# Kernel optimization log

Hardware: AMD Instinct MI355X
Metric: run time of the kernel (lower is better)

## Reference

```python
import jax, jax.numpy as jnp
import numpy as np

EPS_LN1 = 1e-6   # partial(nn.LayerNorm, eps=1e-6)
EPS_OUT = 1e-5   # nn.LayerNorm default inside SS3D out_norm


def _layernorm(x, w, b, eps):
    m = jnp.mean(x, axis=-1, keepdims=True)
    v = jnp.var(x, axis=-1, keepdims=True)
    return (x - m) * jax.lax.rsqrt(v + eps) * w + b


def _selective_scan(dA, dBx):
    # dA, dBx: (B, K, d, L, N); linear recurrence h_t = dA_t * h_{t-1} + dBx_t
    def comb(c1, c2):
        a1, b1 = c1
        a2, b2 = c2
        return a2 * a1, a2 * b1 + b2
    _, hs = jax.lax.associative_scan(comb, (dA, dBx), axis=3)
    return hs  # (B, K, d, L, N)


def setup_inputs() -> dict:
    key = jax.random.key(0)
    ks = jax.random.split(key, 12)
    B, D, H, W, C = 1, 16, 16, 16, 96
    d, N, K, R = 96, 16, 6, 6  # d_inner, d_state, n_scan_dirs, dt_rank
    s = 0.02
    f = lambda k, shp: jax.random.normal(k, shp, dtype=jnp.float32)
    return {
        "x": f(ks[0], (B, D, H, W, C)),
        "ln1_w": jnp.ones((C,), jnp.float32),
        "ln1_b": jnp.zeros((C,), jnp.float32),
        "in_proj_w": f(ks[1], (2 * d, C)) * s,
        "conv_w": f(ks[2], (d, 1, 3, 3, 3)) * s,
        "conv_b": f(ks[3], (d,)) * s,
        "x_proj_w": f(ks[4], (K, R + 2 * N, d)) * s,
        "dt_proj_w": f(ks[5], (K, d, R)) * s,
        "dt_proj_b": f(ks[6], (K, d)) * s,
        "A_log": jnp.log(1.0 + 15.0 * jax.random.uniform(ks[7], (K, d, N), jnp.float32)),
        "D_skip": f(ks[8], (K, d)) * s,
        "out_norm_w": jnp.ones((d,), jnp.float32),
        "out_norm_b": jnp.zeros((d,), jnp.float32),
        "out_proj_w": f(ks[9], (C, d)) * s,
    }


def reference(x, ln1_w, ln1_b, in_proj_w, conv_w, conv_b, x_proj_w,
              dt_proj_w, dt_proj_b, A_log, D_skip, out_norm_w, out_norm_b,
              out_proj_w):
    B, D, H, W, C = x.shape
    L = D * H * W
    K, _, d = x_proj_w.shape
    R = dt_proj_w.shape[2]
    N = A_log.shape[2]

    # pre-norm
    xn = _layernorm(x, ln1_w, ln1_b, EPS_LN1)

    # in_proj -> (x, z)
    xz = jnp.einsum('bdhwc,ec->bdhwe', xn, in_proj_w)  # (B,D,H,W,2d)
    xh, z = jnp.split(xz, 2, axis=-1)

    # depthwise 3x3x3 conv + SiLU, channels-first
    xc = jnp.transpose(xh, (0, 4, 1, 2, 3))  # (B,d,D,H,W)
    xc = jax.lax.conv_general_dilated(
        xc, conv_w, window_strides=(1, 1, 1), padding='SAME',
        dimension_numbers=('NCDHW', 'OIDHW', 'NCDHW'),
        feature_group_count=d)
    xc = jax.nn.silu(xc + conv_b[None, :, None, None, None])

    # K = 6 scan orderings: DHW, HWD, WDH and their reverses
    o0 = xc.reshape(B, d, L)
    o1 = jnp.transpose(xc, (0, 1, 3, 4, 2)).reshape(B, d, L)  # (H,W,D) order
    o2 = jnp.transpose(xc, (0, 1, 4, 2, 3)).reshape(B, d, L)  # (W,D,H) order
    fwd3 = jnp.stack([o0, o1, o2], axis=1)                    # (B,3,d,L)
    xs = jnp.concatenate([fwd3, jnp.flip(fwd3, axis=-1)], axis=1)  # (B,K,d,L)

    # per-direction input-dependent parameters
    x_dbl = jnp.einsum('bkdl,kcd->bkcl', xs, x_proj_w)        # (B,K,R+2N,L)
    dt, Bm, Cm = jnp.split(x_dbl, [R, R + N], axis=2)
    dts = jnp.einsum('bkrl,kdr->bkdl', dt, dt_proj_w) + dt_proj_b[None, :, :, None]
    dts = jax.nn.softplus(dts)                                # delta_softplus

    A = -jnp.exp(A_log)                                       # (K,d,N)
    dA = jnp.exp(dts[..., None] * A[None, :, :, None, :])     # (B,K,d,L,N)
    Bt = jnp.transpose(Bm, (0, 1, 3, 2))                      # (B,K,L,N)
    dBx = (dts * xs)[..., None] * Bt[:, :, None, :, :]        # (B,K,d,L,N)

    hs = _selective_scan(dA, dBx)                             # (B,K,d,L,N)
    Ct = jnp.transpose(Cm, (0, 1, 3, 2))                      # (B,K,L,N)
    ys = jnp.einsum('bkdln,bkln->bkdl', hs, Ct) + D_skip[None, :, :, None] * xs

    # undo reversals and orderings, sum the 6 paths
    yf = ys[:, :3] + jnp.flip(ys[:, 3:], axis=-1)             # (B,3,d,L)
    y0 = yf[:, 0]
    y1 = jnp.transpose(yf[:, 1].reshape(B, d, H, W, D), (0, 1, 4, 2, 3)).reshape(B, d, L)
    y2 = jnp.transpose(yf[:, 2].reshape(B, d, W, D, H), (0, 1, 3, 4, 2)).reshape(B, d, L)
    y = (y0 + y1 + y2).reshape(B, d, D, H, W)
    y = jnp.transpose(y, (0, 2, 3, 4, 1))                     # (B,D,H,W,d)

    # out_norm, gate, out_proj
    y = _layernorm(y, out_norm_w, out_norm_b, EPS_OUT)
    y = y * jax.nn.silu(z)
    out = jnp.einsum('bdhwe,ce->bdhwc', y, out_proj_w)

    # residual (drop_path is identity at eval)
    return x + out
```

## Files before the change

### kernel.cpp

```cpp
#include <hip/hip_runtime.h>
#include <hip/hip_bf16.h>

#define L 4096
#define CDIM 96
#define DDIM 96
#define KDIR 6
#define NST 16
#define RRK 6
#define YSTRIDE 40
#define NCHUNK 256
#define CHLEN 16

typedef _Float16 half4v __attribute__((ext_vector_type(4)));

__device__ __forceinline__ float sigmoidf_(float x) { return 1.f / (1.f + __expf(-x)); }

__device__ __forceinline__ int sigma_k(int kb, int l) {
    if (kb == 0) return l;
    if (kb == 1) return ((l & 15) << 8) | ((l >> 8) << 4) | ((l >> 4) & 15);
    return (((l >> 4) & 15) << 8) | ((l & 15) << 4) | (l >> 8);
}

__global__ void __launch_bounds__(192) k1_ln_inproj(
        const float* __restrict__ x, const float* __restrict__ ln_w,
        const float* __restrict__ ln_b, const float* __restrict__ Wp,
        float* __restrict__ xh_t, float* __restrict__ zs) {
    int s0 = blockIdx.x * 8;
    int tid = threadIdx.x;
    __shared__ __align__(16) float xt[8][96];
    __shared__ __align__(16) float xn[8][96];
    __shared__ float mss[8], rss[8];
    ((float4*)&xt[0][0])[tid] = ((const float4*)(x + (size_t)s0 * 96))[tid];
    __syncthreads();
    int wave = tid >> 6, lane = tid & 63;
    for (int r = wave; r < 8; r += 3) {
        float v = xt[r][lane] + ((lane < 32) ? xt[r][64 + lane] : 0.f);
#pragma unroll
        for (int off = 1; off < 64; off <<= 1) v += __shfl_xor(v, off);
        float vs = xt[r][lane] * xt[r][lane] + ((lane < 32) ? xt[r][64 + lane] * xt[r][64 + lane] : 0.f);
#pragma unroll
        for (int off = 1; off < 64; off <<= 1) vs += __shfl_xor(vs, off);
        if (lane == 0) {
            float mean = v * (1.f / 96.f);
            float var = vs * (1.f / 96.f) - mean * mean;
            mss[r] = mean; rss[r] = rsqrtf(var + 1e-6f);
        }
    }
    __syncthreads();
    {
        int r = tid / 24, c4 = tid % 24;
        float4 xv = ((float4*)&xt[r][0])[c4];
        float4 wv = ((const float4*)ln_w)[c4];
        float4 bv = ((const float4*)ln_b)[c4];
        float m = mss[r], rs = rss[r];
        float4 o;
        o.x = (xv.x - m) * rs * wv.x + bv.x;
        o.y = (xv.y - m) * rs * wv.y + bv.y;
        o.z = (xv.z - m) * rs * wv.z + bv.z;
        o.w = (xv.w - m) * rs * wv.w + bv.w;
        ((float4*)&xn[r][0])[c4] = o;
    }
    float4 Wr[24];
    const float4* wr = (const float4*)(Wp + (size_t)tid * 96);
#pragma unroll
    for (int c4 = 0; c4 < 24; c4++) Wr[c4] = wr[c4];
    __syncthreads();
#pragma unroll
    for (int s = 0; s < 8; s++) {
        const float4* xr4 = (const float4*)&xn[s][0];
        float a0 = 0.f, a1 = 0.f, a2 = 0.f, a3 = 0.f;
#pragma unroll
        for (int c4 = 0; c4 < 24; c4 += 4) {
            float4 x0 = xr4[c4], x1 = xr4[c4 + 1], x2 = xr4[c4 + 2], x3 = xr4[c4 + 3];
            a0 += Wr[c4].x * x0.x + Wr[c4].y * x0.y + Wr[c4].z * x0.z + Wr[c4].w * x0.w;
            a1 += Wr[c4+1].x * x1.x + Wr[c4+1].y * x1.y + Wr[c4+1].z * x1.z + Wr[c4+1].w * x1.w;
            a2 += Wr[c4+2].x * x2.x + Wr[c4+2].y * x2.y + Wr[c4+2].z * x2.z + Wr[c4+2].w * x2.w;
            a3 += Wr[c4+3].x * x3.x + Wr[c4+3].y * x3.y + Wr[c4+3].z * x3.z + Wr[c4+3].w * x3.w;
        }
        float acc = (a0 + a1) + (a2 + a3);
        if (tid < 96) xh_t[(size_t)tid * L + s0 + s] = acc;
        else zs[(size_t)(s0 + s) * 96 + (tid - 96)] = acc * sigmoidf_(acc);
    }
}

__global__ void k2_conv(const float* __restrict__ xh_t, const float* __restrict__ cw,
                        const float* __restrict__ cb, float* __restrict__ xc,
                        float* __restrict__ xcT) {
    int idx = blockIdx.x * 256 + threadIdx.x;
    int c = idx >> 12, s = idx & 4095;
    int dz = s >> 8, h = (s >> 4) & 15, w = s & 15;
    const float* xin = xh_t + c * L;
    const float* wc = cw + c * 27;
    float acc = cb[c];
#pragma unroll
    for (int i = 0; i < 3; i++) {
        int z2 = dz + i - 1; if ((unsigned)z2 > 15u) continue;
#pragma unroll
        for (int j = 0; j < 3; j++) {
            int h2 = h + j - 1; if ((unsigned)h2 > 15u) continue;
#pragma unroll
            for (int kk = 0; kk < 3; kk++) {
                int w2 = w + kk - 1; if ((unsigned)w2 > 15u) continue;
                acc += xin[z2 * 256 + h2 * 16 + w2] * wc[i * 9 + j * 3 + kk];
            }
        }
    }
    float r = acc * sigmoidf_(acc);
    xc[c * L + s] = r;
    xcT[s * 96 + c] = r;
}

__global__ void k3_xproj(const float* __restrict__ xc, const float* __restrict__ Wx,
                         const float* __restrict__ Wdt, const float* __restrict__ bdt,
                         float* __restrict__ Y2, float* __restrict__ Zs) {
    int k = blockIdx.x;
    int tid = threadIdx.x;
    int sbase = blockIdx.y * 256;
    int s = sbase + tid;
    int ch = blockIdx.z;
    int base = (ch < 2) ? ch * 10 : 20 + (ch - 2) * 9;
    int cnt = (ch < 2) ? 10 : 9;
    __shared__ float dts[256][6];
    float acc[10];
#pragma unroll
    for (int i = 0; i < 10; i++) acc[i] = 0.f;
    const float* wk = Wx + ((size_t)k * (RRK + 2 * NST) + base) * DDIM;
    for (int dd = 0; dd < 96; dd += 4) {
        float v[4];
#pragma unroll
        for (int j = 0; j < 4; j++) v[j] = xc[(dd + j) * L + s];
#pragma unroll
        for (int j = 0; j < 4; j++)
#pragma unroll
            for (int i = 0; i < 10; i++) acc[i] += wk[i * DDIM + dd + j] * v[j];
    }
    float* yo = Y2 + ((size_t)k * L + s) * YSTRIDE;
#pragma unroll
    for (int i = 0; i < 10; i++) {
        if (i < cnt) {
            int c = base + i;
            if (c >= 6) yo[c + 2] = acc[i];
        }
    }
    if (ch == 0) {
#pragma unroll
        for (int r = 0; r < 6; r++) dts[tid][r] = acc[r];
        __syncthreads();
        for (int i = 0; i < 96; i++) {
            int idx = i * 256 + tid;
            int d = idx % 96;
            int sr = idx / 96;
            const float* wr = Wdt + ((size_t)k * 96 + d) * 6;
            float a = bdt[k * 96 + d];
#pragma unroll
            for (int r = 0; r < 6; r++) a += wr[r] * dts[sr][r];
            float sp = (a > 15.f) ? a : __logf(1.f + __expf(a));
            Zs[((size_t)k * L + sbase + sr) * 96 + d] = sp;
        }
    }
}


__global__ void __launch_bounds__(256) ka_scan(
        const float* __restrict__ Zs, const float* __restrict__ xcT,
        const float* __restrict__ Y2, const float* __restrict__ A_log,
        _Float16* __restrict__ Aah, _Float16* __restrict__ Abh) {
    int t = blockIdx.x * 256 + threadIdx.x;
    int nq = t & 3;
    int q = t >> 2;
    int d = q % 96;
    int rest = q / 96;
    int chunk = rest % NCHUNK;
    int k = rest / NCHUNK;
    int kb = (k < 3) ? k : (k - 3);
    bool flip = (k >= 3);
    float An[4];
    {
        float4 al = *(const float4*)(A_log + ((size_t)k * 96 + d) * 16 + nq * 4);
        An[0] = -__expf(al.x); An[1] = -__expf(al.y);
        An[2] = -__expf(al.z); An[3] = -__expf(al.w);
    }
    float a[4] = {1.f, 1.f, 1.f, 1.f};
    float b[4] = {0.f, 0.f, 0.f, 0.f};
    const float* Zk = Zs + (size_t)k * L * 96;
    const float* Yk = Y2 + (size_t)k * L * YSTRIDE;
    int l0 = chunk * CHLEN;
    for (int i = 0; i < CHLEN; i += 4) {
        int sI[4]; float dt[4], xv[4]; float4 Bv[4];
#pragma unroll
        for (int j = 0; j < 4; j++) {
            int l = l0 + i + j;
            int lp = flip ? (4095 - l) : l;
            sI[j] = sigma_k(kb, lp);
        }
#pragma unroll
        for (int j = 0; j < 4; j++) {
            dt[j] = Zk[(size_t)sI[j] * 96 + d];
            xv[j] = xcT[(size_t)sI[j] * 96 + d];
            Bv[j] = *(const float4*)(Yk + (size_t)sI[j] * YSTRIDE + 8 + nq * 4);
        }
#pragma unroll
        for (int j = 0; j < 4; j++) {
            float dtx = dt[j] * xv[j];
            float e0 = __expf(dt[j] * An[0]);
            float e1 = __expf(dt[j] * An[1]);
            float e2 = __expf(dt[j] * An[2]);
            float e3 = __expf(dt[j] * An[3]);
            b[0] = e0 * b[0] + dtx * Bv[j].x; a[0] *= e0;
            b[1] = e1 * b[1] + dtx * Bv[j].y; a[1] *= e1;
            b[2] = e2 * b[2] + dtx * Bv[j].z; a[2] *= e2;
            b[3] = e3 * b[3] + dtx * Bv[j].w; a[3] *= e3;
        }
    }
    size_t o = (((size_t)k * NCHUNK + chunk) * 96 + d) * 16 + nq * 4;
    half4v ha, hb;
    ha.x = (_Float16)a[0]; ha.y = (_Float16)a[1]; ha.z = (_Float16)a[2]; ha.w = (_Float16)a[3];
    hb.x = (_Float16)b[0]; hb.y = (_Float16)b[1]; hb.z = (_Float16)b[2]; hb.w = (_Float16)b[3];
    *(half4v*)(Aah + o) = ha;
    *(half4v*)(Abh + o) = hb;
}

__global__ void __launch_bounds__(256) kb_combine(
        const _Float16* __restrict__ Aah, const _Float16* __restrict__ Abh,
        _Float16* __restrict__ Pbh) {
    int t = blockIdx.x * 256 + threadIdx.x;
    int n = t & 15;
    int rest = t >> 4;
    int d = rest % 96;
    int k = rest / 96;
    size_t base = ((size_t)k * NCHUNK * 96 + d) * 16 + n;
    const size_t cstride = 96 * 16;
    float rb = 0.f;
    for (int c0 = 0; c0 < NCHUNK; c0 += 16) {
        float av[16], bv[16];
#pragma unroll
        for (int j = 0; j < 16; j++) {
            av[j] = (float)Aah[base + (size_t)(c0 + j) * cstride];
            bv[j] = (float)Abh[base + (size_t)(c0 + j) * cstride];
        }
#pragma unroll
        for (int j = 0; j < 16; j++) {
            Pbh[base + (size_t)(c0 + j) * cstride] = (_Float16)rb;
            rb = av[j] * rb + bv[j];
        }
    }
}

__global__ void __launch_bounds__(256) kc_apply(
        const float* __restrict__ Zs, const float* __restrict__ xcT,
        const float* __restrict__ Y2, const float* __restrict__ A_log,
        const float* __restrict__ D_skip, const _Float16* __restrict__ Pbh,
        float* __restrict__ ys_buf) {
    int t = blockIdx.x * 256 + threadIdx.x;
    int nq = t & 3;
    int q = t >> 2;
    int d = q % 96;
    int rest = q / 96;
    int chunk = rest % NCHUNK;
    int k = rest / NCHUNK;
    int kb = (k < 3) ? k : (k - 3);
    bool flip = (k >= 3);
    float An[4];
    {
        float4 al = *(const float4*)(A_log + ((size_t)k * 96 + d) * 16 + nq * 4);
        An[0] = -__expf(al.x); An[1] = -__expf(al.y);
        An[2] = -__expf(al.z); An[3] = -__expf(al.w);
    }
    float Dk = D_skip[k * DDIM + d];
    float h[4];
    {
        half4v hp = *(const half4v*)(Pbh + (((size_t)k * NCHUNK + chunk) * 96 + d) * 16 + nq * 4);
        h[0] = (float)hp.x; h[1] = (float)hp.y; h[2] = (float)hp.z; h[3] = (float)hp.w;
    }
    const float* Zk = Zs + (size_t)k * L * 96;
    const float* Yk = Y2 + (size_t)k * L * YSTRIDE;
    float* ysk = ys_buf + (size_t)k * L * 96;
    int l0 = chunk * CHLEN;
    for (int i = 0; i < CHLEN; i += 4) {
        int sI[4]; float dt[4], xv[4]; float4 Bv[4], Cv[4];
#pragma unroll
        for (int j = 0; j < 4; j++) {
            int l = l0 + i + j;
            int lp = flip ? (4095 - l) : l;
            sI[j] = sigma_k(kb, lp);
        }
#pragma unroll
        for (int j = 0; j < 4; j++) {
            dt[j] = Zk[(size_t)sI[j] * 96 + d];
            xv[j] = xcT[(size_t)sI[j] * 96 + d];
            Bv[j] = *(const float4*)(Yk + (size_t)sI[j] * YSTRIDE + 8 + nq * 4);
            Cv[j] = *(const float4*)(Yk + (size_t)sI[j] * YSTRIDE + 24 + nq * 4);
        }
#pragma unroll
        for (int j = 0; j < 4; j++) {
            float dtx = dt[j] * xv[j];
            float e0 = __expf(dt[j] * An[0]);
            float e1 = __expf(dt[j] * An[1]);
            float e2 = __expf(dt[j] * An[2]);
            float e3 = __expf(dt[j] * An[3]);
            h[0] = e0 * h[0] + dtx * Bv[j].x;
            h[1] = e1 * h[1] + dtx * Bv[j].y;
            h[2] = e2 * h[2] + dtx * Bv[j].z;
            h[3] = e3 * h[3] + dtx * Bv[j].w;
            float p = h[0] * Cv[j].x + h[1] * Cv[j].y + h[2] * Cv[j].z + h[3] * Cv[j].w;
            p += __shfl_xor(p, 1);
            p += __shfl_xor(p, 2);
            if (nq == 0) ysk[(size_t)sI[j] * 96 + d] = p + Dk * xv[j];
        }
    }
}

__global__ void __launch_bounds__(192) k6_out(
        const float* __restrict__ ys_buf, const float* __restrict__ zs,
        const float* __restrict__ onw, const float* __restrict__ onb,
        const float* __restrict__ Wo, const float* __restrict__ x,
        float* __restrict__ out) {
    int s0 = blockIdx.x * 16;
    int tid = threadIdx.x;
    __shared__ __align__(16) float vt[16][96];
    __shared__ __align__(16) float gt[16][96];
    __shared__ float mss[16], rss[16];
#pragma unroll
    for (int j = 0; j < 8; j++) {
        int f = tid + j * 192;
        int sr = f / 96, c = f % 96;
        float v = 0.f;
#pragma unroll
        for (int k = 0; k < KDIR; k++)
            v += ys_buf[((size_t)k * L + s0 + sr) * 96 + c];
        vt[sr][c] = v;
    }
    __syncthreads();
    int wave = tid >> 6, lane = tid & 63;
    for (int r = wave; r < 16; r += 3) {
        float v = vt[r][lane] + ((lane < 32) ? vt[r][64 + lane] : 0.f);
#pragma unroll
        for (int off = 1; off < 64; off <<= 1) v += __shfl_xor(v, off);
        float vs = vt[r][lane] * vt[r][lane] + ((lane < 32) ? vt[r][64 + lane] * vt[r][64 + lane] : 0.f);
#pragma unroll
        for (int off = 1; off < 64; off <<= 1) vs += __shfl_xor(vs, off);
        if (lane == 0) {
            float mean = v * (1.f / 96.f);
            float var = vs * (1.f / 96.f) - mean * mean;
            mss[r] = mean; rss[r] = rsqrtf(var + 1e-5f);
        }
    }
    __syncthreads();
#pragma unroll
    for (int j = 0; j < 8; j++) {
        int f = tid + j * 192;
        int sr = f / 96, c = f % 96;
        float g = (vt[sr][c] - mss[sr]) * rss[sr] * onw[c] + onb[c];
        gt[sr][c] = g * zs[(size_t)(s0 + sr) * 96 + c];
    }
    int e = tid % 96, sg = tid / 96;
    float4 Wr[24];
    const float4* wr = (const float4*)(Wo + (size_t)e * 96);
#pragma unroll
    for (int c4 = 0; c4 < 24; c4++) Wr[c4] = wr[c4];
    __syncthreads();
#pragma unroll
    for (int j = 0; j < 8; j++) {
        int s = sg * 8 + j;
        const float4* g4 = (const float4*)&gt[s][0];
        float a0 = 0.f, a1 = 0.f, a2 = 0.f, a3 = 0.f;
#pragma unroll
        for (int c4 = 0; c4 < 24; c4 += 4) {
            float4 x0 = g4[c4], x1 = g4[c4 + 1], x2 = g4[c4 + 2], x3 = g4[c4 + 3];
            a0 += Wr[c4].x * x0.x + Wr[c4].y * x0.y + Wr[c4].z * x0.z + Wr[c4].w * x0.w;
            a1 += Wr[c4+1].x * x1.x + Wr[c4+1].y * x1.y + Wr[c4+1].z * x1.z + Wr[c4+1].w * x1.w;
            a2 += Wr[c4+2].x * x2.x + Wr[c4+2].y * x2.y + Wr[c4+2].z * x2.z + Wr[c4+2].w * x2.w;
            a3 += Wr[c4+3].x * x3.x + Wr[c4+3].y * x3.y + Wr[c4+3].z * x3.z + Wr[c4+3].w * x3.w;
        }
        float acc = (a0 + a1) + (a2 + a3) + x[(size_t)(s0 + s) * 96 + e];
        out[(size_t)(s0 + s) * 96 + e] = acc;
    }
}

extern "C" void kernel_launch(void* const* d_in, const int* in_sizes, int n_in,
                              void* d_out, int out_size, void* d_ws, size_t ws_size,
                              hipStream_t stream) {
    const float* x        = (const float*)d_in[0];
    const float* ln1_w    = (const float*)d_in[1];
    const float* ln1_b    = (const float*)d_in[2];
    const float* in_proj  = (const float*)d_in[3];
    const float* conv_w   = (const float*)d_in[4];
    const float* conv_b   = (const float*)d_in[5];
    const float* x_proj   = (const float*)d_in[6];
    const float* dt_w     = (const float*)d_in[7];
    const float* dt_b     = (const float*)d_in[8];
    const float* A_log    = (const float*)d_in[9];
    const float* D_skip   = (const float*)d_in[10];
    const float* onw      = (const float*)d_in[11];
    const float* onb      = (const float*)d_in[12];
    const float* out_w    = (const float*)d_in[13];
    float* out = (float*)d_out;

    float* xh_t = (float*)d_ws;
    float* zs   = xh_t + 96 * L;
    float* xc   = zs + 96 * L;
    float* xcT  = xc + 96 * L;
    float* Y2   = xcT + 96 * L;
    float* Zs   = Y2 + (size_t)KDIR * L * YSTRIDE;
    float* ysb  = Zs + (size_t)KDIR * L * DDIM;
    _Float16* Aah = (_Float16*)(ysb + (size_t)KDIR * L * DDIM);
    _Float16* Abh = Aah + (size_t)KDIR * NCHUNK * DDIM * NST;
    _Float16* Pbh = Abh + (size_t)KDIR * NCHUNK * DDIM * NST;

    k1_ln_inproj<<<dim3(L / 8), dim3(192), 0, stream>>>(x, ln1_w, ln1_b, in_proj, xh_t, zs);
    k2_conv<<<dim3(96 * L / 256), dim3(256), 0, stream>>>(xh_t, conv_w, conv_b, xc, xcT);
    k3_xproj<<<dim3(KDIR, 16, 4), dim3(256), 0, stream>>>(xc, x_proj, dt_w, dt_b, Y2, Zs);
    ka_scan<<<dim3(KDIR * NCHUNK * DDIM * 4 / 256), dim3(256), 0, stream>>>(Zs, xcT, Y2, A_log, Aah, Abh);
    kb_combine<<<dim3(KDIR * DDIM * NST / 256), dim3(256), 0, stream>>>(Aah, Abh, Pbh);
    kc_apply<<<dim3(KDIR * NCHUNK * DDIM * 4 / 256), dim3(256), 0, stream>>>(Zs, xcT, Y2, A_log, D_skip, Pbh, ysb);
    k6_out<<<dim3(L / 16), dim3(192), 0, stream>>>(ysb, zs, onw, onb, out_w, x, out);
}
```

Baseline: 194.7 us.

## Store intermediate activations in fp16 and interleave scan outputs per position

Result: faster. 189.9 us (-2.4%).

```diff
diff --git a/kernel.cpp b/kernel.cpp
--- a/kernel.cpp
+++ b/kernel.cpp
@@ -7,7 +7,7 @@
 #define KDIR 6
 #define NST 16
 #define RRK 6
-#define YSTRIDE 40
+#define YH 32
 #define NCHUNK 256
 #define CHLEN 16
 
@@ -24,7 +24,7 @@
 __global__ void __launch_bounds__(192) k1_ln_inproj(
         const float* __restrict__ x, const float* __restrict__ ln_w,
         const float* __restrict__ ln_b, const float* __restrict__ Wp,
-        float* __restrict__ xh_t, float* __restrict__ zs) {
+        _Float16* __restrict__ xhh, _Float16* __restrict__ zsh) {
     int s0 = blockIdx.x * 8;
     int tid = threadIdx.x;
     __shared__ __align__(16) float xt[8][96];
@@ -78,18 +78,18 @@
             a3 += Wr[c4+3].x * x3.x + Wr[c4+3].y * x3.y + Wr[c4+3].z * x3.z + Wr[c4+3].w * x3.w;
         }
         float acc = (a0 + a1) + (a2 + a3);
-        if (tid < 96) xh_t[(size_t)tid * L + s0 + s] = acc;
-        else zs[(size_t)(s0 + s) * 96 + (tid - 96)] = acc * sigmoidf_(acc);
-    }
-}
-
-__global__ void k2_conv(const float* __restrict__ xh_t, const float* __restrict__ cw,
-                        const float* __restrict__ cb, float* __restrict__ xc,
-                        float* __restrict__ xcT) {
+        if (tid < 96) xhh[(size_t)tid * L + s0 + s] = (_Float16)acc;
+        else zsh[(size_t)(s0 + s) * 96 + (tid - 96)] = (_Float16)(acc * sigmoidf_(acc));
+    }
+}
+
+__global__ void k2_conv(const _Float16* __restrict__ xhh, const float* __restrict__ cw,
+                        const float* __restrict__ cb, _Float16* __restrict__ xch,
+                        _Float16* __restrict__ xcTh) {
     int idx = blockIdx.x * 256 + threadIdx.x;
     int c = idx >> 12, s = idx & 4095;
     int dz = s >> 8, h = (s >> 4) & 15, w = s & 15;
-    const float* xin = xh_t + c * L;
+    const _Float16* xin = xhh + (size_t)c * L;
     const float* wc = cw + c * 27;
     float acc = cb[c];
 #pragma unroll
@@ -101,18 +101,19 @@
 #pragma unroll
             for (int kk = 0; kk < 3; kk++) {
                 int w2 = w + kk - 1; if ((unsigned)w2 > 15u) continue;
-                acc += xin[z2 * 256 + h2 * 16 + w2] * wc[i * 9 + j * 3 + kk];
+                acc += (float)xin[z2 * 256 + h2 * 16 + w2] * wc[i * 9 + j * 3 + kk];
             }
         }
     }
     float r = acc * sigmoidf_(acc);
-    xc[c * L + s] = r;
-    xcT[s * 96 + c] = r;
-}
-
-__global__ void k3_xproj(const float* __restrict__ xc, const float* __restrict__ Wx,
+    _Float16 hr = (_Float16)r;
+    xch[(size_t)c * L + s] = hr;
+    xcTh[(size_t)s * 96 + c] = hr;
+}
+
+__global__ void k3_xproj(const _Float16* __restrict__ xch, const float* __restrict__ Wx,
                          const float* __restrict__ Wdt, const float* __restrict__ bdt,
-                         float* __restrict__ Y2, float* __restrict__ Zs) {
+                         _Float16* __restrict__ Y2h, _Float16* __restrict__ Zsh) {
     int k = blockIdx.x;
     int tid = threadIdx.x;
     int sbase = blockIdx.y * 256;
@@ -128,18 +129,18 @@
     for (int dd = 0; dd < 96; dd += 4) {
         float v[4];
 #pragma unroll
-        for (int j = 0; j < 4; j++) v[j] = xc[(dd + j) * L + s];
+        for (int j = 0; j < 4; j++) v[j] = (float)xch[(size_t)(dd + j) * L + s];
 #pragma unroll
         for (int j = 0; j < 4; j++)
 #pragma unroll
             for (int i = 0; i < 10; i++) acc[i] += wk[i * DDIM + dd + j] * v[j];
     }
-    float* yo = Y2 + ((size_t)k * L + s) * YSTRIDE;
+    _Float16* yo = Y2h + ((size_t)k * L + s) * YH;
 #pragma unroll
     for (int i = 0; i < 10; i++) {
         if (i < cnt) {
             int c = base + i;
-            if (c >= 6) yo[c + 2] = acc[i];
+            if (c >= 6) yo[c - 6] = (_Float16)acc[i];
         }
     }
     if (ch == 0) {
@@ -155,15 +156,15 @@
 #pragma unroll
             for (int r = 0; r < 6; r++) a += wr[r] * dts[sr][r];
             float sp = (a > 15.f) ? a : __logf(1.f + __expf(a));
-            Zs[((size_t)k * L + sbase + sr) * 96 + d] = sp;
+            Zsh[((size_t)k * L + sbase + sr) * 96 + d] = (_Float16)sp;
         }
     }
 }
 
 
 __global__ void __launch_bounds__(256) ka_scan(
-        const float* __restrict__ Zs, const float* __restrict__ xcT,
-        const float* __restrict__ Y2, const float* __restrict__ A_log,
+        const _Float16* __restrict__ Zsh, const _Float16* __restrict__ xcTh,
+        const _Float16* __restrict__ Y2h, const float* __restrict__ A_log,
         _Float16* __restrict__ Aah, _Float16* __restrict__ Abh) {
     int t = blockIdx.x * 256 + threadIdx.x;
     int nq = t & 3;
@@ -182,11 +183,11 @@
     }
     float a[4] = {1.f, 1.f, 1.f, 1.f};
     float b[4] = {0.f, 0.f, 0.f, 0.f};
-    const float* Zk = Zs + (size_t)k * L * 96;
-    const float* Yk = Y2 + (size_t)k * L * YSTRIDE;
+    const _Float16* Zk = Zsh + (size_t)k * L * 96;
+    const _Float16* Yk = Y2h + (size_t)k * L * YH;
     int l0 = chunk * CHLEN;
     for (int i = 0; i < CHLEN; i += 4) {
-        int sI[4]; float dt[4], xv[4]; float4 Bv[4];
+        int sI[4]; float dt[4], xv[4]; half4v Bh[4];
 #pragma unroll
         for (int j = 0; j < 4; j++) {
             int l = l0 + i + j;
@@ -195,9 +196,9 @@
         }
 #pragma unroll
         for (int j = 0; j < 4; j++) {
-            dt[j] = Zk[(size_t)sI[j] * 96 + d];
-            xv[j] = xcT[(size_t)sI[j] * 96 + d];
-            Bv[j] = *(const float4*)(Yk + (size_t)sI[j] * YSTRIDE + 8 + nq * 4);
+            dt[j] = (float)Zk[(size_t)sI[j] * 96 + d];
+            xv[j] = (float)xcTh[(size_t)sI[j] * 96 + d];
+            Bh[j] = *(const half4v*)(Yk + (size_t)sI[j] * YH + nq * 4);
         }
 #pragma unroll
         for (int j = 0; j < 4; j++) {
@@ -206,10 +207,10 @@
             float e1 = __expf(dt[j] * An[1]);
             float e2 = __expf(dt[j] * An[2]);
             float e3 = __expf(dt[j] * An[3]);
-            b[0] = e0 * b[0] + dtx * Bv[j].x; a[0] *= e0;
-            b[1] = e1 * b[1] + dtx * Bv[j].y; a[1] *= e1;
-            b[2] = e2 * b[2] + dtx * Bv[j].z; a[2] *= e2;
-            b[3] = e3 * b[3] + dtx * Bv[j].w; a[3] *= e3;
+            b[0] = e0 * b[0] + dtx * (float)Bh[j].x; a[0] *= e0;
+            b[1] = e1 * b[1] + dtx * (float)Bh[j].y; a[1] *= e1;
+            b[2] = e2 * b[2] + dtx * (float)Bh[j].z; a[2] *= e2;
+            b[3] = e3 * b[3] + dtx * (float)Bh[j].w; a[3] *= e3;
         }
     }
     size_t o = (((size_t)k * NCHUNK + chunk) * 96 + d) * 16 + nq * 4;
@@ -247,10 +248,10 @@
 }
 
 __global__ void __launch_bounds__(256) kc_apply(
-        const float* __restrict__ Zs, const float* __restrict__ xcT,
-        const float* __restrict__ Y2, const float* __restrict__ A_log,
+        const _Float16* __restrict__ Zsh, const _Float16* __restrict__ xcTh,
+        const _Float16* __restrict__ Y2h, const float* __restrict__ A_log,
         const float* __restrict__ D_skip, const _Float16* __restrict__ Pbh,
-        float* __restrict__ ys_buf) {
+        _Float16* __restrict__ ysh) {
     int t = blockIdx.x * 256 + threadIdx.x;
     int nq = t & 3;
     int q = t >> 2;
@@ -272,12 +273,11 @@
         half4v hp = *(const half4v*)(Pbh + (((size_t)k * NCHUNK + chunk) * 96 + d) * 16 + nq * 4);
         h[0] = (float)hp.x; h[1] = (float)hp.y; h[2] = (float)hp.z; h[3] = (float)hp.w;
     }
-    const float* Zk = Zs + (size_t)k * L * 96;
-    const float* Yk = Y2 + (size_t)k * L * YSTRIDE;
-    float* ysk = ys_buf + (size_t)k * L * 96;
+    const _Float16* Zk = Zsh + (size_t)k * L * 96;
+    const _Float16* Yk = Y2h + (size_t)k * L * YH;
     int l0 = chunk * CHLEN;
     for (int i = 0; i < CHLEN; i += 4) {
-        int sI[4]; float dt[4], xv[4]; float4 Bv[4], Cv[4];
+        int sI[4]; float dt[4], xv[4]; half4v Bh[4], Ch[4];
 #pragma unroll
         for (int j = 0; j < 4; j++) {
             int l = l0 + i + j;
@@ -286,10 +286,10 @@
         }
 #pragma unroll
         for (int j = 0; j < 4; j++) {
-            dt[j] = Zk[(size_t)sI[j] * 96 + d];
-            xv[j] = xcT[(size_t)sI[j] * 96 + d];
-            Bv[j] = *(const float4*)(Yk + (size_t)sI[j] * YSTRIDE + 8 + nq * 4);
-            Cv[j] = *(const float4*)(Yk + (size_t)sI[j] * YSTRIDE + 24 + nq * 4);
+            dt[j] = (float)Zk[(size_t)sI[j] * 96 + d];
+            xv[j] = (float)xcTh[(size_t)sI[j] * 96 + d];
+            Bh[j] = *(const half4v*)(Yk + (size_t)sI[j] * YH + nq * 4);
+            Ch[j] = *(const half4v*)(Yk + (size_t)sI[j] * YH + 16 + nq * 4);
         }
 #pragma unroll
         for (int j = 0; j < 4; j++) {
@@ -298,41 +298,42 @@
             float e1 = __expf(dt[j] * An[1]);
             float e2 = __expf(dt[j] * An[2]);
             float e3 = __expf(dt[j] * An[3]);
-            h[0] = e0 * h[0] + dtx * Bv[j].x;
-            h[1] = e1 * h[1] + dtx * Bv[j].y;
-            h[2] = e2 * h[2] + dtx * Bv[j].z;
-            h[3] = e3 * h[3] + dtx * Bv[j].w;
-            float p = h[0] * Cv[j].x + h[1] * Cv[j].y + h[2] * Cv[j].z + h[3] * Cv[j].w;
+            h[0] = e0 * h[0] + dtx * (float)Bh[j].x;
+            h[1] = e1 * h[1] + dtx * (float)Bh[j].y;
+            h[2] = e2 * h[2] + dtx * (float)Bh[j].z;
+            h[3] = e3 * h[3] + dtx * (float)Bh[j].w;
+            float p = h[0] * (float)Ch[j].x + h[1] * (float)Ch[j].y
+                    + h[2] * (float)Ch[j].z + h[3] * (float)Ch[j].w;
             p += __shfl_xor(p, 1);
             p += __shfl_xor(p, 2);
-            if (nq == 0) ysk[(size_t)sI[j] * 96 + d] = p + Dk * xv[j];
+            if (nq == 0) ysh[((size_t)sI[j] * KDIR + k) * 96 + d] = (_Float16)(p + Dk * xv[j]);
         }
     }
 }
 
 __global__ void __launch_bounds__(192) k6_out(
-        const float* __restrict__ ys_buf, const float* __restrict__ zs,
+        const _Float16* __restrict__ ysh, const _Float16* __restrict__ zsh,
         const float* __restrict__ onw, const float* __restrict__ onb,
         const float* __restrict__ Wo, const float* __restrict__ x,
         float* __restrict__ out) {
-    int s0 = blockIdx.x * 16;
+    int s0 = blockIdx.x * 8;
     int tid = threadIdx.x;
-    __shared__ __align__(16) float vt[16][96];
-    __shared__ __align__(16) float gt[16][96];
-    __shared__ float mss[16], rss[16];
-#pragma unroll
-    for (int j = 0; j < 8; j++) {
+    __shared__ __align__(16) float vt[8][96];
+    __shared__ __align__(16) float gt[8][96];
+    __shared__ float mss[8], rss[8];
+#pragma unroll
+    for (int j = 0; j < 4; j++) {
         int f = tid + j * 192;
         int sr = f / 96, c = f % 96;
+        const _Float16* yr = ysh + ((size_t)(s0 + sr) * KDIR) * 96 + c;
         float v = 0.f;
 #pragma unroll
-        for (int k = 0; k < KDIR; k++)
-            v += ys_buf[((size_t)k * L + s0 + sr) * 96 + c];
+        for (int k = 0; k < KDIR; k++) v += (float)yr[k * 96];
         vt[sr][c] = v;
     }
     __syncthreads();
     int wave = tid >> 6, lane = tid & 63;
-    for (int r = wave; r < 16; r += 3) {
+    for (int r = wave; r < 8; r += 3) {
         float v = vt[r][lane] + ((lane < 32) ? vt[r][64 + lane] : 0.f);
 #pragma unroll
         for (int off = 1; off < 64; off <<= 1) v += __shfl_xor(v, off);
@@ -347,11 +348,11 @@
     }
     __syncthreads();
 #pragma unroll
-    for (int j = 0; j < 8; j++) {
+    for (int j = 0; j < 4; j++) {
         int f = tid + j * 192;
         int sr = f / 96, c = f % 96;
         float g = (vt[sr][c] - mss[sr]) * rss[sr] * onw[c] + onb[c];
-        gt[sr][c] = g * zs[(size_t)(s0 + sr) * 96 + c];
+        gt[sr][c] = g * (float)zsh[(size_t)(s0 + sr) * 96 + c];
     }
     int e = tid % 96, sg = tid / 96;
     float4 Wr[24];
@@ -360,8 +361,8 @@
     for (int c4 = 0; c4 < 24; c4++) Wr[c4] = wr[c4];
     __syncthreads();
 #pragma unroll
-    for (int j = 0; j < 8; j++) {
-        int s = sg * 8 + j;
+    for (int j = 0; j < 4; j++) {
+        int s = sg * 4 + j;
         const float4* g4 = (const float4*)&gt[s][0];
         float a0 = 0.f, a1 = 0.f, a2 = 0.f, a3 = 0.f;
 #pragma unroll
@@ -396,22 +397,22 @@
     const float* out_w    = (const float*)d_in[13];
     float* out = (float*)d_out;
 
-    float* xh_t = (float*)d_ws;
-    float* zs   = xh_t + 96 * L;
-    float* xc   = zs + 96 * L;
-    float* xcT  = xc + 96 * L;
-    float* Y2   = xcT + 96 * L;
-    float* Zs   = Y2 + (size_t)KDIR * L * YSTRIDE;
-    float* ysb  = Zs + (size_t)KDIR * L * DDIM;
-    _Float16* Aah = (_Float16*)(ysb + (size_t)KDIR * L * DDIM);
-    _Float16* Abh = Aah + (size_t)KDIR * NCHUNK * DDIM * NST;
-    _Float16* Pbh = Abh + (size_t)KDIR * NCHUNK * DDIM * NST;
-
-    k1_ln_inproj<<<dim3(L / 8), dim3(192), 0, stream>>>(x, ln1_w, ln1_b, in_proj, xh_t, zs);
-    k2_conv<<<dim3(96 * L / 256), dim3(256), 0, stream>>>(xh_t, conv_w, conv_b, xc, xcT);
-    k3_xproj<<<dim3(KDIR, 16, 4), dim3(256), 0, stream>>>(xc, x_proj, dt_w, dt_b, Y2, Zs);
-    ka_scan<<<dim3(KDIR * NCHUNK * DDIM * 4 / 256), dim3(256), 0, stream>>>(Zs, xcT, Y2, A_log, Aah, Abh);
+    _Float16* xhh  = (_Float16*)d_ws;
+    _Float16* zsh  = xhh + (size_t)96 * L;
+    _Float16* xch  = zsh + (size_t)96 * L;
+    _Float16* xcTh = xch + (size_t)96 * L;
+    _Float16* Y2h  = xcTh + (size_t)96 * L;
+    _Float16* Zsh  = Y2h + (size_t)KDIR * L * YH;
+    _Float16* ysh  = Zsh + (size_t)KDIR * L * 96;
+    _Float16* Aah  = ysh + (size_t)L * KDIR * 96;
+    _Float16* Abh  = Aah + (size_t)KDIR * NCHUNK * DDIM * NST;
+    _Float16* Pbh  = Abh + (size_t)KDIR * NCHUNK * DDIM * NST;
+
+    k1_ln_inproj<<<dim3(L / 8), dim3(192), 0, stream>>>(x, ln1_w, ln1_b, in_proj, xhh, zsh);
+    k2_conv<<<dim3(96 * L / 256), dim3(256), 0, stream>>>(xhh, conv_w, conv_b, xch, xcTh);
+    k3_xproj<<<dim3(KDIR, 16, 4), dim3(256), 0, stream>>>(xch, x_proj, dt_w, dt_b, Y2h, Zsh);
+    ka_scan<<<dim3(KDIR * NCHUNK * DDIM * 4 / 256), dim3(256), 0, stream>>>(Zsh, xcTh, Y2h, A_log, Aah, Abh);
     kb_combine<<<dim3(KDIR * DDIM * NST / 256), dim3(256), 0, stream>>>(Aah, Abh, Pbh);
-    kc_apply<<<dim3(KDIR * NCHUNK * DDIM * 4 / 256), dim3(256), 0, stream>>>(Zs, xcT, Y2, A_log, D_skip, Pbh, ysb);
-    k6_out<<<dim3(L / 16), dim3(192), 0, stream>>>(ysb, zs, onw, onb, out_w, x, out);
-}
+    kc_apply<<<dim3(KDIR * NCHUNK * DDIM * 4 / 256), dim3(256), 0, stream>>>(Zsh, xcTh, Y2h, A_log, D_skip, Pbh, ysh);
+    k6_out<<<dim3(L / 8), dim3(192), 0, stream>>>(ysh, zsh, onw, onb, out_w, x, out);
+}
```
